# Kernel optimization log

Hardware: AMD Instinct MI355X
Metric: run time of the kernel (lower is better)

Reference implementation:

```python
import jax, jax.numpy as jnp
import numpy as np

N = 50000      # num_nodes
SEQ = 52       # seq_len (weeks)
FIN = 16       # in_channels
H = 128        # hidden_dim
E = 800000     # num edges (before self-loops)
NEG_SLOPE = 0.2


def setup_inputs() -> dict:
    key = jax.random.key(0)
    ks = jax.random.split(key, 10)
    return {
        "x_seq": jax.random.normal(ks[0], (SEQ, N, FIN), jnp.float32),
        "edge_index": jax.random.randint(ks[1], (2, E), 0, N),
        "Wg": jax.random.normal(ks[2], (FIN, H), jnp.float32) * 0.1,       # GAT linear (no bias on lin in PyG default path; bias added at end)
        "att_src": jax.random.normal(ks[3], (H,), jnp.float32) * 0.1,
        "att_dst": jax.random.normal(ks[4], (H,), jnp.float32) * 0.1,
        "bias_g": jnp.zeros((H,), jnp.float32),
        "W_ih": jax.random.normal(ks[5], (3 * H, H), jnp.float32) * 0.05,  # GRUCell input weights (r,z,n order)
        "W_hh": jax.random.normal(ks[6], (3 * H, H), jnp.float32) * 0.05,
        "b_ih": jnp.zeros((3 * H,), jnp.float32),
        "b_hh": jnp.zeros((3 * H,), jnp.float32),
        "W_fc": jax.random.normal(ks[7], (1, H), jnp.float32) * 0.1,
        "b_fc": jnp.zeros((1,), jnp.float32),
    }


def _gat(x, src, dst, Wg, att_src, att_dst, bias_g):
    # x: [N, FIN] -> xp: [N, H]
    xp = x @ Wg
    a_s = xp @ att_src  # [N]
    a_d = xp @ att_dst  # [N]
    e = jax.nn.leaky_relu(a_s[src] + a_d[dst], NEG_SLOPE)          # [E+N] edge scores
    m = jax.ops.segment_max(e, dst, num_segments=N)                # softmax over incoming edges per dst
    w = jnp.exp(e - m[dst])
    denom = jax.ops.segment_sum(w, dst, num_segments=N)
    alpha = w / denom[dst]
    out = jax.ops.segment_sum(alpha[:, None] * xp[src], dst, num_segments=N)  # [N, H]
    return out + bias_g


def _gru_cell(x, h, W_ih, W_hh, b_ih, b_hh):
    gi = x @ W_ih.T + b_ih  # [N, 3H]
    gh = h @ W_hh.T + b_hh
    i_r, i_z, i_n = jnp.split(gi, 3, axis=1)
    h_r, h_z, h_n = jnp.split(gh, 3, axis=1)
    r = jax.nn.sigmoid(i_r + h_r)
    z = jax.nn.sigmoid(i_z + h_z)
    n = jnp.tanh(i_n + r * h_n)
    return (1.0 - z) * n + z * h


def reference(x_seq, edge_index, Wg, att_src, att_dst, bias_g, W_ih, W_hh, b_ih, b_hh, W_fc, b_fc):
    # PyG GATConv add_self_loops=True
    loop = jnp.arange(N)
    src = jnp.concatenate([edge_index[0], loop])
    dst = jnp.concatenate([edge_index[1], loop])

    def step(h, xt):
        spatial = jax.nn.relu(_gat(xt, src, dst, Wg, att_src, att_dst, bias_g))
        h_new = _gru_cell(spatial, h, W_ih, W_hh, b_ih, b_hh)
        return h_new, None

    h0 = jnp.zeros((N, H), jnp.float32)
    hT, _ = jax.lax.scan(step, h0, x_seq)
    return hT @ W_fc.T + b_fc  # [N, 1]
```

## Files before the change

kernel.cpp:

```cpp
#include <hip/hip_runtime.h>
#include <math.h>

#define NN 50000
#define SEQ 52
#define FIN 16
#define HD 128
#define NEG_SLOPE 0.2f

typedef short bf16x8 __attribute__((ext_vector_type(8)));
typedef float f32x16 __attribute__((ext_vector_type(16)));

__device__ __forceinline__ short f2bf(float x) {
    unsigned u = __float_as_uint(x);
    u += 0x7fffu + ((u >> 16) & 1u);
    return (short)(u >> 16);
}
__device__ __forceinline__ float b2f(short s) {
    return __uint_as_float(((unsigned)(unsigned short)s) << 16);
}

__global__ void deg_init_kernel(int* deg, int n) {
    int i = blockIdx.x * blockDim.x + threadIdx.x;
    if (i < n) deg[i] = 1;
}

__global__ void deg_count_kernel(const int* __restrict__ dst, int* deg, int e) {
    int i = blockIdx.x * blockDim.x + threadIdx.x;
    if (i < e) atomicAdd(&deg[dst[i]], 1);
}

__global__ __launch_bounds__(1024) void scan_kernel(const int* __restrict__ deg,
                                                    int* row_ptr, int n) {
    __shared__ int buf[1024];
    __shared__ int carry;
    int tid = threadIdx.x;
    if (tid == 0) carry = 0;
    __syncthreads();
    for (int base = 0; base < n; base += 1024) {
        int i = base + tid;
        int v = (i < n) ? deg[i] : 0;
        buf[tid] = v;
        __syncthreads();
        for (int off = 1; off < 1024; off <<= 1) {
            int t = (tid >= off) ? buf[tid - off] : 0;
            __syncthreads();
            buf[tid] += t;
            __syncthreads();
        }
        if (i < n) row_ptr[i] = carry + buf[tid] - v;
        __syncthreads();
        if (tid == 1023) carry += buf[1023];
        __syncthreads();
    }
    if (tid == 0) row_ptr[n] = carry;
}

__global__ void selfloop_kernel(const int* __restrict__ row_ptr, int* cursor,
                                int* col, int n) {
    int i = blockIdx.x * blockDim.x + threadIdx.x;
    if (i < n) {
        int p = row_ptr[i];
        col[p] = i;
        cursor[i] = p + 1;
    }
}

__global__ void scatter_kernel(const int* __restrict__ src, const int* __restrict__ dst,
                               int* cursor, int* col, int e) {
    int i = blockIdx.x * blockDim.x + threadIdx.x;
    if (i < e) {
        int p = atomicAdd(&cursor[dst[i]], 1);
        col[p] = src[i];
    }
}

__global__ void wpack_kernel(const float* __restrict__ Wi, const float* __restrict__ Wh,
                             short* __restrict__ wfrag) {
    int idx = blockIdx.x * blockDim.x + threadIdx.x;
    if (idx >= 3 * 4 * 8 * 4 * 64) return;
    int lane = idx & 63;
    int which = (idx >> 6) & 3;
    int ks = (idx >> 8) & 7;
    int slab = (idx >> 11) & 3;
    int g = idx >> 13;
    int col = slab * 32 + (lane & 31);
    int kcol = ks * 16 + (lane >> 5) * 8;
    const float* Wsrc = (which < 2) ? Wi : Wh;
    const float* row = Wsrc + (size_t)(g * HD + col) * HD + kcol;
    short* dstp = wfrag + (size_t)idx * 8;
    bool lo = (which & 1);
#pragma unroll
    for (int e = 0; e < 8; ++e) {
        float v = row[e];
        short hi = f2bf(v);
        dstp[e] = lo ? f2bf(v - b2f(hi)) : hi;
    }
}


__global__ __launch_bounds__(256) void xp_kernel(
    const float* __restrict__ x, const float* __restrict__ Wg,
    const float* __restrict__ att_src, const float* __restrict__ att_dst,
    unsigned* __restrict__ xpb, float* __restrict__ a_s, float* __restrict__ a_d, int n) {
    int wave = (blockIdx.x * blockDim.x + threadIdx.x) >> 6;
    int lane = threadIdx.x & 63;
    if (wave >= n) return;
    const float* xr = x + (size_t)wave * FIN;
    float xv[FIN];
#pragma unroll
    for (int k = 0; k < FIN; ++k) xv[k] = xr[k];
    int c0 = 2 * lane, c1 = 2 * lane + 1;
    float v0 = 0.f, v1 = 0.f;
#pragma unroll
    for (int k = 0; k < FIN; ++k) {
        v0 += xv[k] * Wg[k * HD + c0];
        v1 += xv[k] * Wg[k * HD + c1];
    }
    unsigned p = (unsigned)(unsigned short)f2bf(v0) |
                 ((unsigned)(unsigned short)f2bf(v1) << 16);
    xpb[(size_t)wave * 64 + lane] = p;
    float s = v0 * att_src[c0] + v1 * att_src[c1];
    float d = v0 * att_dst[c0] + v1 * att_dst[c1];
#pragma unroll
    for (int off = 32; off; off >>= 1) {
        s += __shfl_xor(s, off);
        d += __shfl_xor(d, off);
    }
    if (lane == 0) { a_s[wave] = s; a_d[wave] = d; }
}

__global__ __launch_bounds__(256, 2) void gatgru_kernel(
    const int* __restrict__ row_ptr, const int* __restrict__ col,
    const float* __restrict__ a_s, const float* __restrict__ a_d,
    const short* __restrict__ xpb, const float* __restrict__ bias_g,
    float* __restrict__ h, const short* __restrict__ wfrag,
    const float* __restrict__ b_ih, const float* __restrict__ b_hh, int n) {
    __shared__ bf16x8 sSH[512];
    __shared__ bf16x8 sSL[512];
    __shared__ bf16x8 sHH[512];
    __shared__ bf16x8 sHL[512];

    int t = threadIdx.x;
    int lane = t & 63;
    int w = t >> 6;
    int n0 = blockIdx.x * 32;

    float h8[2][8];
#pragma unroll
    for (int q = 0; q < 2; ++q) {
        int ks = w * 2 + q;
        int row = n0 + (lane & 31);
        if (row >= n) row = n - 1;
        int kcol = ks * 16 + (lane >> 5) * 8;
        const float* hp = h + (size_t)row * HD + kcol;
        *(float4*)(h8[q]) = *(const float4*)(hp);
        *(float4*)(h8[q] + 4) = *(const float4*)(hp + 4);
    }

    int g = t >> 4;
    int fg = t & 15;
    int glane = lane & 0x30;

#pragma unroll
    for (int nn = 0; nn < 2; ++nn) {
        int nl = g + nn * 16;
        int nd = n0 + nl;
        int sidx = (fg >> 1) * 64 + (fg & 1) * 32 + nl;
        if (nd < n) {
            int start = row_ptr[nd], end = row_ptr[nd + 1];
            float ad = a_d[nd];
            float acc[8] = {0.f, 0.f, 0.f, 0.f, 0.f, 0.f, 0.f, 0.f};
            float dpart = 0.f;
            for (int base = start; base < end; base += 16) {
                int cnt = end - base;
                if (cnt > 16) cnt = 16;
                int s = 0;
                float wgt = 0.f;
                if (fg < cnt) {
                    s = col[base + fg];
                    float e = a_s[s] + ad;
                    e = (e > 0.f) ? e : NEG_SLOPE * e;
                    wgt = __expf(e);
                }
                dpart += wgt;
                for (int k = 0; k < cnt; k += 4) {
                    int si[4];
                    float wt[4];
#pragma unroll
                    for (int u = 0; u < 4; ++u) {
                        int c = k + u;
                        int cc = (c < cnt) ? c : 0;
                        si[u] = __shfl(s, glane | cc);
                        wt[u] = __shfl(wgt, glane | cc);
                        if (c >= cnt) wt[u] = 0.f;
                    }
                    bf16x8 r[4];
#pragma unroll
                    for (int u = 0; u < 4; ++u)
                        r[u] = *(const bf16x8*)(xpb + (size_t)si[u] * HD + fg * 8);
#pragma unroll
                    for (int u = 0; u < 4; ++u)
#pragma unroll
                        for (int j = 0; j < 8; ++j) acc[j] += wt[u] * b2f(r[u][j]);
                }
            }
            dpart += __shfl_xor(dpart, 8);
            dpart += __shfl_xor(dpart, 4);
            dpart += __shfl_xor(dpart, 2);
            dpart += __shfl_xor(dpart, 1);
            float inv = __fdividef(1.f, dpart);
            bf16x8 sh, sl;
#pragma unroll
            for (int j = 0; j < 8; ++j) {
                float o = acc[j] * inv + bias_g[fg * 8 + j];
                o = fmaxf(o, 0.f);
                short hi = f2bf(o);
                sh[j] = hi;
                sl[j] = f2bf(o - b2f(hi));
            }
            sSH[sidx] = sh;
            sSL[sidx] = sl;
        } else {
            bf16x8 z;
#pragma unroll
            for (int j = 0; j < 8; ++j) z[j] = 0;
            sSH[sidx] = z;
            sSL[sidx] = z;
        }
    }

#pragma unroll
    for (int q = 0; q < 2; ++q) {
        int ks = w * 2 + q;
        bf16x8 hh, hl;
#pragma unroll
        for (int j = 0; j < 8; ++j) {
            short b = f2bf(h8[q][j]);
            hh[j] = b;
            hl[j] = f2bf(h8[q][j] - b2f(b));
        }
        int li = ks * 64 + lane;
        sHH[li] = hh;
        sHL[li] = hl;
    }
    __syncthreads();

    int j0 = w * 32;
    int cj = lane & 31;
    int kh = lane >> 5;

    f32x16 arz[2], ain, ahn;
#pragma unroll
    for (int r = 0; r < 16; ++r) {
        arz[0][r] = 0.f; arz[1][r] = 0.f; ain[r] = 0.f; ahn[r] = 0.f;
    }

    const short* wb = wfrag + (size_t)w * 16384 + (size_t)lane * 8;

    bf16x8 wv[3][12];
#pragma unroll
    for (int p = 0; p < 2; ++p) {
#pragma unroll
        for (int gg = 0; gg < 3; ++gg) {
#pragma unroll
            for (int q = 0; q < 4; ++q)
                wv[p][gg * 4 + q] = *(const bf16x8*)(wb + gg * 65536 + p * 2048 + q * 512);
        }
    }

#pragma unroll
    for (int ks = 0; ks < 8; ++ks) {
        int cur = ks % 3;
        if (ks < 6) {
            int nxt = (ks + 2) % 3;
#pragma unroll
            for (int gg = 0; gg < 3; ++gg) {
#pragma unroll
                for (int q = 0; q < 4; ++q)
                    wv[nxt][gg * 4 + q] =
                        *(const bf16x8*)(wb + gg * 65536 + (ks + 2) * 2048 + q * 512);
            }
        }
        int li = ks * 64 + lane;
        bf16x8 aSH = sSH[li];
        bf16x8 aSL = sSL[li];
        bf16x8 aHH = sHH[li];
        bf16x8 aHL = sHL[li];
#pragma unroll
        for (int gg = 0; gg < 2; ++gg) {
            bf16x8 wih = wv[cur][gg * 4 + 0];
            bf16x8 wil = wv[cur][gg * 4 + 1];
            bf16x8 whh = wv[cur][gg * 4 + 2];
            bf16x8 whl = wv[cur][gg * 4 + 3];
            arz[gg] = __builtin_amdgcn_mfma_f32_32x32x16_bf16(aSH, wih, arz[gg], 0, 0, 0);
            arz[gg] = __builtin_amdgcn_mfma_f32_32x32x16_bf16(aHH, whh, arz[gg], 0, 0, 0);
            arz[gg] = __builtin_amdgcn_mfma_f32_32x32x16_bf16(aSL, wih, arz[gg], 0, 0, 0);
            arz[gg] = __builtin_amdgcn_mfma_f32_32x32x16_bf16(aHL, whh, arz[gg], 0, 0, 0);
            arz[gg] = __builtin_amdgcn_mfma_f32_32x32x16_bf16(aSH, wil, arz[gg], 0, 0, 0);
            arz[gg] = __builtin_amdgcn_mfma_f32_32x32x16_bf16(aHH, whl, arz[gg], 0, 0, 0);
        }
        {
            bf16x8 wih = wv[cur][8];
            bf16x8 wil = wv[cur][9];
            bf16x8 whh = wv[cur][10];
            bf16x8 whl = wv[cur][11];
            ain = __builtin_amdgcn_mfma_f32_32x32x16_bf16(aSH, wih, ain, 0, 0, 0);
            ahn = __builtin_amdgcn_mfma_f32_32x32x16_bf16(aHH, whh, ahn, 0, 0, 0);
            ain = __builtin_amdgcn_mfma_f32_32x32x16_bf16(aSL, wih, ain, 0, 0, 0);
            ahn = __builtin_amdgcn_mfma_f32_32x32x16_bf16(aHL, whh, ahn, 0, 0, 0);
            ain = __builtin_amdgcn_mfma_f32_32x32x16_bf16(aSH, wil, ain, 0, 0, 0);
            ahn = __builtin_amdgcn_mfma_f32_32x32x16_bf16(aHH, whl, ahn, 0, 0, 0);
        }
    }

    int j = j0 + cj;
    float brz0 = b_ih[j] + b_hh[j];
    float brz1 = b_ih[HD + j] + b_hh[HD + j];
    float bin_ = b_ih[2 * HD + j];
    float bhn = b_hh[2 * HD + j];
    const short* hhs = (const short*)sHH;
    const short* hls = (const short*)sHL;
    int ksj = j >> 4, halfj = (j >> 3) & 1, ej = j & 7;

#pragma unroll
    for (int r = 0; r < 16; ++r) {
        int nl = (r & 3) + 8 * (r >> 2) + 4 * kh;
        int node = n0 + nl;
        if (node < n) {
            float rr = __fdividef(1.f, 1.f + __expf(-(arz[0][r] + brz0)));
            float zz = __fdividef(1.f, 1.f + __expf(-(arz[1][r] + brz1)));
            float u = ain[r] + bin_ + rr * (ahn[r] + bhn);
            float ex = __expf(2.f * u);
            float nn2 = 1.f - __fdividef(2.f, ex + 1.f);
            int li = (ksj * 64 + nl + 32 * halfj) * 8 + ej;
            float hold = b2f(hhs[li]) + b2f(hls[li]);
            h[(size_t)node * HD + j] = (1.f - zz) * nn2 + zz * hold;
        }
    }
}

__global__ __launch_bounds__(256) void fc_kernel(
    const float* __restrict__ h, const float* __restrict__ W_fc,
    const float* __restrict__ b_fc, float* __restrict__ out, int n) {
    int wave = (blockIdx.x * blockDim.x + threadIdx.x) >> 6;
    int lane = threadIdx.x & 63;
    if (wave >= n) return;
    float v = h[(size_t)wave * HD + lane] * W_fc[lane] +
              h[(size_t)wave * HD + lane + 64] * W_fc[lane + 64];
#pragma unroll
    for (int off = 32; off; off >>= 1) v += __shfl_xor(v, off);
    if (lane == 0) out[wave] = v + b_fc[0];
}

extern "C" void kernel_launch(void* const* d_in, const int* in_sizes, int n_in,
                              void* d_out, int out_size, void* d_ws, size_t ws_size,
                              hipStream_t stream) {
    const float* x_seq   = (const float*)d_in[0];
    const int*   ei      = (const int*)d_in[1];
    const float* Wg      = (const float*)d_in[2];
    const float* att_src = (const float*)d_in[3];
    const float* att_dst = (const float*)d_in[4];
    const float* bias_g  = (const float*)d_in[5];
    const float* W_ih    = (const float*)d_in[6];
    const float* W_hh    = (const float*)d_in[7];
    const float* b_ih    = (const float*)d_in[8];
    const float* b_hh    = (const float*)d_in[9];
    const float* W_fc    = (const float*)d_in[10];
    const float* b_fc    = (const float*)d_in[11];
    float* out = (float*)d_out;

    const int N = NN;
    const int E = in_sizes[1] / 2;
    const int* src = ei;
    const int* dst = ei + E;

    char* w = (char*)d_ws;
    size_t off = 0;
    auto alloc = [&](size_t bytes) {
        char* p = w + off;
        off = (off + bytes + 255) & ~(size_t)255;
        return p;
    };
    int*   deg     = (int*)alloc((size_t)N * 4);
    int*   row_ptr = (int*)alloc((size_t)(N + 1) * 4);
    int*   cursor  = (int*)alloc((size_t)N * 4);
    int*   col     = (int*)alloc((size_t)(E + N) * 4);
    float* a_s     = (float*)alloc((size_t)N * 4);
    float* a_d     = (float*)alloc((size_t)N * 4);
    unsigned* xpb  = (unsigned*)alloc((size_t)N * 64 * 4);
    float* hbuf    = (float*)alloc((size_t)N * HD * 4);
    short* wfrag   = (short*)alloc((size_t)3 * 4 * 8 * 4 * 64 * 8 * 2);

    hipMemsetAsync(hbuf, 0, (size_t)N * HD * 4, stream);

    deg_init_kernel<<<(N + 255) / 256, 256, 0, stream>>>(deg, N);
    deg_count_kernel<<<(E + 255) / 256, 256, 0, stream>>>(dst, deg, E);
    scan_kernel<<<1, 1024, 0, stream>>>(deg, row_ptr, N);
    selfloop_kernel<<<(N + 255) / 256, 256, 0, stream>>>(row_ptr, cursor, col, N);
    scatter_kernel<<<(E + 255) / 256, 256, 0, stream>>>(src, dst, cursor, col, E);
    wpack_kernel<<<(24576 + 255) / 256, 256, 0, stream>>>(W_ih, W_hh, wfrag);

    int node_wave_blocks = (N * 64 + 255) / 256;
    int fused_blocks = (N + 31) / 32;

    for (int t = 0; t < SEQ; ++t) {
        const float* xt = x_seq + (size_t)t * N * FIN;
        xp_kernel<<<node_wave_blocks, 256, 0, stream>>>(xt, Wg, att_src, att_dst,
                                                        xpb, a_s, a_d, N);
        gatgru_kernel<<<fused_blocks, 256, 0, stream>>>(row_ptr, col, a_s, a_d,
                                                        (const short*)xpb, bias_g,
                                                        hbuf, wfrag, b_ih, b_hh, N);
    }
    fc_kernel<<<node_wave_blocks, 256, 0, stream>>>(hbuf, W_fc, b_fc, out, N);
}
```

Measured before the change: 6.299 ms.

## Precompute edge weights per block and issue all 16 neighbor gathers together

Adds a per-edge destination array built during CSR construction. Each gatgru block first computes the exp attention weights for all edges of its 32 nodes in a flat, fully parallel pass and writes them to global memory. The aggregation loop then reads these weights and issues up to 16 neighbor feature loads at once before accumulating, to get more memory-level parallelism than the old groups of 4. The cost is an extra global write and read of the weights, a barrier, and higher register pressure from 16 bf16x8 buffers under launch_bounds(256,2).

After: 6.888 ms. +9.3%, slower.

```diff
diff --git a/kernel.cpp b/kernel.cpp
--- a/kernel.cpp
+++ b/kernel.cpp
@@ -56,21 +56,24 @@
 }
 
 __global__ void selfloop_kernel(const int* __restrict__ row_ptr, int* cursor,
-                                int* col, int n) {
+                                int* col, int* dst_slot, int n) {
     int i = blockIdx.x * blockDim.x + threadIdx.x;
     if (i < n) {
         int p = row_ptr[i];
         col[p] = i;
+        dst_slot[p] = i;
         cursor[i] = p + 1;
     }
 }
 
 __global__ void scatter_kernel(const int* __restrict__ src, const int* __restrict__ dst,
-                               int* cursor, int* col, int e) {
+                               int* cursor, int* col, int* dst_slot, int e) {
     int i = blockIdx.x * blockDim.x + threadIdx.x;
     if (i < e) {
-        int p = atomicAdd(&cursor[dst[i]], 1);
+        int d = dst[i];
+        int p = atomicAdd(&cursor[d], 1);
         col[p] = src[i];
+        dst_slot[p] = d;
     }
 }
 
@@ -131,6 +134,7 @@
 
 __global__ __launch_bounds__(256, 2) void gatgru_kernel(
     const int* __restrict__ row_ptr, const int* __restrict__ col,
+    const int* __restrict__ dst_slot, float* __restrict__ wgt_g,
     const float* __restrict__ a_s, const float* __restrict__ a_d,
     const short* __restrict__ xpb, const float* __restrict__ bias_g,
     float* __restrict__ h, const short* __restrict__ wfrag,
@@ -157,6 +161,16 @@
         *(float4*)(h8[q] + 4) = *(const float4*)(hp + 4);
     }
 
+    int nend = (n0 + 32 < n) ? (n0 + 32) : n;
+    int rp0 = row_ptr[n0];
+    int rp1 = row_ptr[nend];
+    for (int p = rp0 + t; p < rp1; p += 256) {
+        float e = a_s[col[p]] + a_d[dst_slot[p]];
+        e = (e > 0.f) ? e : NEG_SLOPE * e;
+        wgt_g[p] = __expf(e);
+    }
+    __syncthreads();
+
     int g = t >> 4;
     int fg = t & 15;
     int glane = lane & 0x30;
@@ -168,40 +182,33 @@
         int sidx = (fg >> 1) * 64 + (fg & 1) * 32 + nl;
         if (nd < n) {
             int start = row_ptr[nd], end = row_ptr[nd + 1];
-            float ad = a_d[nd];
             float acc[8] = {0.f, 0.f, 0.f, 0.f, 0.f, 0.f, 0.f, 0.f};
             float dpart = 0.f;
             for (int base = start; base < end; base += 16) {
                 int cnt = end - base;
                 if (cnt > 16) cnt = 16;
                 int s = 0;
-                float wgt = 0.f;
+                float wi = 0.f;
                 if (fg < cnt) {
                     s = col[base + fg];
-                    float e = a_s[s] + ad;
-                    e = (e > 0.f) ? e : NEG_SLOPE * e;
-                    wgt = __expf(e);
+                    wi = wgt_g[base + fg];
                 }
-                dpart += wgt;
-                for (int k = 0; k < cnt; k += 4) {
-                    int si[4];
-                    float wt[4];
-#pragma unroll
-                    for (int u = 0; u < 4; ++u) {
-                        int c = k + u;
-                        int cc = (c < cnt) ? c : 0;
-                        si[u] = __shfl(s, glane | cc);
-                        wt[u] = __shfl(wgt, glane | cc);
-                        if (c >= cnt) wt[u] = 0.f;
+                dpart += wi;
+                bf16x8 r[16];
+#pragma unroll
+                for (int u = 0; u < 16; ++u) {
+                    if (u < cnt) {
+                        int si = __shfl(s, glane | u);
+                        r[u] = *(const bf16x8*)(xpb + (size_t)si * HD + fg * 8);
                     }
-                    bf16x8 r[4];
-#pragma unroll
-                    for (int u = 0; u < 4; ++u)
-                        r[u] = *(const bf16x8*)(xpb + (size_t)si[u] * HD + fg * 8);
-#pragma unroll
-                    for (int u = 0; u < 4; ++u)
-#pragma unroll
-                        for (int j = 0; j < 8; ++j) acc[j] += wt[u] * b2f(r[u][j]);
+                }
+#pragma unroll
+                for (int u = 0; u < 16; ++u) {
+                    if (u < cnt) {
+                        float wu = __shfl(wi, glane | u);
+#pragma unroll
+                        for (int j = 0; j < 8; ++j) acc[j] += wu * b2f(r[u][j]);
+                    }
                 }
             }
             dpart += __shfl_xor(dpart, 8);
@@ -381,23 +388,27 @@
         off = (off + bytes + 255) & ~(size_t)255;
         return p;
     };
-    int*   deg     = (int*)alloc((size_t)N * 4);
-    int*   row_ptr = (int*)alloc((size_t)(N + 1) * 4);
-    int*   cursor  = (int*)alloc((size_t)N * 4);
-    int*   col     = (int*)alloc((size_t)(E + N) * 4);
-    float* a_s     = (float*)alloc((size_t)N * 4);
-    float* a_d     = (float*)alloc((size_t)N * 4);
-    unsigned* xpb  = (unsigned*)alloc((size_t)N * 64 * 4);
-    float* hbuf    = (float*)alloc((size_t)N * HD * 4);
-    short* wfrag   = (short*)alloc((size_t)3 * 4 * 8 * 4 * 64 * 8 * 2);
+    int*   deg      = (int*)alloc((size_t)N * 4);
+    int*   row_ptr  = (int*)alloc((size_t)(N + 1) * 4);
+    int*   cursor   = (int*)alloc((size_t)N * 4);
+    int*   col      = (int*)alloc((size_t)(E + N) * 4);
+    int*   dst_slot = (int*)alloc((size_t)(E + N) * 4);
+    float* wgt_g    = (float*)alloc((size_t)(E + N) * 4);
+    float* a_s      = (float*)alloc((size_t)N * 4);
+    float* a_d      = (float*)alloc((size_t)N * 4);
+    unsigned* xpb   = (unsigned*)alloc((size_t)N * 64 * 4);
+    float* hbuf     = (float*)alloc((size_t)N * HD * 4);
+    short* wfrag    = (short*)alloc((size_t)3 * 4 * 8 * 4 * 64 * 8 * 2);
 
     hipMemsetAsync(hbuf, 0, (size_t)N * HD * 4, stream);
 
     deg_init_kernel<<<(N + 255) / 256, 256, 0, stream>>>(deg, N);
     deg_count_kernel<<<(E + 255) / 256, 256, 0, stream>>>(dst, deg, E);
     scan_kernel<<<1, 1024, 0, stream>>>(deg, row_ptr, N);
-    selfloop_kernel<<<(N + 255) / 256, 256, 0, stream>>>(row_ptr, cursor, col, N);
-    scatter_kernel<<<(E + 255) / 256, 256, 0, stream>>>(src, dst, cursor, col, E);
+    selfloop_kernel<<<(N + 255) / 256, 256, 0, stream>>>(row_ptr, cursor, col,
+                                                         dst_slot, N);
+    scatter_kernel<<<(E + 255) / 256, 256, 0, stream>>>(src, dst, cursor, col,
+                                                        dst_slot, E);
     wpack_kernel<<<(24576 + 255) / 256, 256, 0, stream>>>(W_ih, W_hh, wfrag);
 
     int node_wave_blocks = (N * 64 + 255) / 256;
@@ -407,7 +418,8 @@
         const float* xt = x_seq + (size_t)t * N * FIN;
         xp_kernel<<<node_wave_blocks, 256, 0, stream>>>(xt, Wg, att_src, att_dst,
                                                         xpb, a_s, a_d, N);
-        gatgru_kernel<<<fused_blocks, 256, 0, stream>>>(row_ptr, col, a_s, a_d,
+        gatgru_kernel<<<fused_blocks, 256, 0, stream>>>(row_ptr, col, dst_slot,
+                                                        wgt_g, a_s, a_d,
                                                         (const short*)xpb, bias_g,
                                                         hbuf, wfrag, b_ih, b_hh, N);
     }
```

## Fuse next-step GAT projection into GAT-GRU kernel with double-buffered xp

Applied to the files above, without the earlier changes.

Computes the next timestep's x@Wg projection, bf16 packing and attention scalars at the tail of the fused GAT-GRU kernel, writing into double-buffered xp/a_s/a_d arrays. This removes 51 separate xp_kernel launches and their launch gaps. In exchange it adds per-thread scalar matmul work (16x16 MACs per thread, with Wg read from global/cache) and register pressure to a kernel bounded to 2 blocks per CU, which could reduce occupancy.

Result: faster. 6.125 ms (-2.8%).

```diff
diff --git a/kernel.cpp b/kernel.cpp
--- a/kernel.cpp
+++ b/kernel.cpp
@@ -134,7 +134,11 @@
     const float* __restrict__ a_s, const float* __restrict__ a_d,
     const short* __restrict__ xpb, const float* __restrict__ bias_g,
     float* __restrict__ h, const short* __restrict__ wfrag,
-    const float* __restrict__ b_ih, const float* __restrict__ b_hh, int n) {
+    const float* __restrict__ b_ih, const float* __restrict__ b_hh, int n,
+    const float* __restrict__ x_next, const float* __restrict__ Wg,
+    const float* __restrict__ att_src, const float* __restrict__ att_dst,
+    unsigned* __restrict__ xpb_next, float* __restrict__ a_s_next,
+    float* __restrict__ a_d_next) {
     __shared__ bf16x8 sSH[512];
     __shared__ bf16x8 sSL[512];
     __shared__ bf16x8 sHH[512];
@@ -337,6 +341,39 @@
             h[(size_t)node * HD + j] = (1.f - zz) * nn2 + zz * hold;
         }
     }
+
+    if (x_next != nullptr) {
+        int node = n0 + (t >> 3);
+        int sub = t & 7;
+        if (node < n) {
+            const float* xr = x_next + (size_t)node * FIN;
+            float xv[FIN];
+#pragma unroll
+            for (int k = 0; k < FIN; ++k) xv[k] = xr[k];
+            float s = 0.f, d = 0.f;
+            unsigned pk[8];
+#pragma unroll
+            for (int c = 0; c < 16; c += 2) {
+                int c0 = sub * 16 + c, c1 = c0 + 1;
+                float v0 = 0.f, v1 = 0.f;
+#pragma unroll
+                for (int k = 0; k < FIN; ++k) {
+                    v0 += xv[k] * Wg[k * HD + c0];
+                    v1 += xv[k] * Wg[k * HD + c1];
+                }
+                s += v0 * att_src[c0] + v1 * att_src[c1];
+                d += v0 * att_dst[c0] + v1 * att_dst[c1];
+                pk[c >> 1] = (unsigned)(unsigned short)f2bf(v0) |
+                             ((unsigned)(unsigned short)f2bf(v1) << 16);
+            }
+            unsigned* dstw = xpb_next + (size_t)node * 64 + sub * 8;
+            *(uint4*)(dstw) = make_uint4(pk[0], pk[1], pk[2], pk[3]);
+            *(uint4*)(dstw + 4) = make_uint4(pk[4], pk[5], pk[6], pk[7]);
+            s += __shfl_xor(s, 1); s += __shfl_xor(s, 2); s += __shfl_xor(s, 4);
+            d += __shfl_xor(d, 1); d += __shfl_xor(d, 2); d += __shfl_xor(d, 4);
+            if (sub == 0) { a_s_next[node] = s; a_d_next[node] = d; }
+        }
+    }
 }
 
 __global__ __launch_bounds__(256) void fc_kernel(
@@ -385,11 +422,18 @@
     int*   row_ptr = (int*)alloc((size_t)(N + 1) * 4);
     int*   cursor  = (int*)alloc((size_t)N * 4);
     int*   col     = (int*)alloc((size_t)(E + N) * 4);
-    float* a_s     = (float*)alloc((size_t)N * 4);
-    float* a_d     = (float*)alloc((size_t)N * 4);
-    unsigned* xpb  = (unsigned*)alloc((size_t)N * 64 * 4);
+    float* a_s0    = (float*)alloc((size_t)N * 4);
+    float* a_d0    = (float*)alloc((size_t)N * 4);
+    float* a_s1    = (float*)alloc((size_t)N * 4);
+    float* a_d1    = (float*)alloc((size_t)N * 4);
+    unsigned* xpb0 = (unsigned*)alloc((size_t)N * 64 * 4);
+    unsigned* xpb1 = (unsigned*)alloc((size_t)N * 64 * 4);
     float* hbuf    = (float*)alloc((size_t)N * HD * 4);
     short* wfrag   = (short*)alloc((size_t)3 * 4 * 8 * 4 * 64 * 8 * 2);
+
+    unsigned* xpbs[2] = {xpb0, xpb1};
+    float* a_ss[2] = {a_s0, a_s1};
+    float* a_ds[2] = {a_d0, a_d1};
 
     hipMemsetAsync(hbuf, 0, (size_t)N * HD * 4, stream);
 
@@ -403,13 +447,17 @@
     int node_wave_blocks = (N * 64 + 255) / 256;
     int fused_blocks = (N + 31) / 32;
 
+    xp_kernel<<<node_wave_blocks, 256, 0, stream>>>(x_seq, Wg, att_src, att_dst,
+                                                    xpb0, a_s0, a_d0, N);
+
     for (int t = 0; t < SEQ; ++t) {
-        const float* xt = x_seq + (size_t)t * N * FIN;
-        xp_kernel<<<node_wave_blocks, 256, 0, stream>>>(xt, Wg, att_src, att_dst,
-                                                        xpb, a_s, a_d, N);
-        gatgru_kernel<<<fused_blocks, 256, 0, stream>>>(row_ptr, col, a_s, a_d,
-                                                        (const short*)xpb, bias_g,
-                                                        hbuf, wfrag, b_ih, b_hh, N);
+        int cur = t & 1, nxt = cur ^ 1;
+        const float* xnext = (t + 1 < SEQ) ? (x_seq + (size_t)(t + 1) * N * FIN)
+                                           : nullptr;
+        gatgru_kernel<<<fused_blocks, 256, 0, stream>>>(
+            row_ptr, col, a_ss[cur], a_ds[cur], (const short*)xpbs[cur], bias_g,
+            hbuf, wfrag, b_ih, b_hh, N,
+            xnext, Wg, att_src, att_dst, xpbs[nxt], a_ss[nxt], a_ds[nxt]);
     }
     fc_kernel<<<node_wave_blocks, 256, 0, stream>>>(hbuf, W_fc, b_fc, out, N);
 }
```
